# Kernel optimization log

Measured on AMD Instinct MI355X. Metric: run time of the kernel, lower is better.

## Reference

```python
import jax, jax.numpy as jnp
import numpy as np

EMBED_DIM = 768
ATTN_DIM = 64


def setup_inputs() -> dict:
    key = jax.random.key(0)
    k1, k2, k3, k4 = jax.random.split(key, 4)
    embedded = jax.random.normal(k1, (4, 4096, EMBED_DIM), dtype=jnp.float32)
    # nn.Linear(embed, attn, bias=False).weight has shape [attn, embed]; y = x @ W.T
    scale = 1.0 / np.sqrt(EMBED_DIM)
    Wq = jax.random.uniform(k2, (ATTN_DIM, EMBED_DIM), dtype=jnp.float32, minval=-scale, maxval=scale)
    Wk = jax.random.uniform(k3, (ATTN_DIM, EMBED_DIM), dtype=jnp.float32, minval=-scale, maxval=scale)
    Wv = jax.random.uniform(k4, (ATTN_DIM, EMBED_DIM), dtype=jnp.float32, minval=-scale, maxval=scale)
    return {"embedded": embedded, "Wq": Wq, "Wk": Wk, "Wv": Wv}


def reference(embedded, Wq, Wk, Wv):
    # Q, K, V: [b, s, a]
    Q = jnp.einsum('bse,ae->bsa', embedded, Wq)
    K = jnp.einsum('bse,ae->bsa', embedded, Wk)
    V = jnp.einsum('bse,ae->bsa', embedded, Wv)
    attn_dim = K.shape[2]
    scores = jnp.einsum('bqa,bka->bqk', Q, K) / jnp.sqrt(jnp.float32(attn_dim))
    s = scores.shape[1]
    # causal mask: positions above the diagonal get -inf
    causal = jnp.tril(jnp.ones((s, s), dtype=bool))
    scores = jnp.where(causal, scores, -jnp.inf)
    probs = jax.nn.softmax(scores, axis=2)
    out = jnp.einsum('bqk,bka->bqa', probs, V)
    return jnp.round(out, 4)
```

## Files before the change

kernel.cpp:

```cpp
#include <hip/hip_runtime.h>
#include <hip/hip_bf16.h>
#include <math.h>

#define EMBED  768
#define SEQ    4096
#define ADIM   64
#define NBATCH 4
#define QSCALE (0.125f * 1.44269504088896340736f)

typedef __bf16 bf16;
typedef unsigned int u32;
typedef __attribute__((ext_vector_type(8))) __bf16 bf16x8;
typedef __attribute__((ext_vector_type(4))) __bf16 bf16x4;
typedef __attribute__((ext_vector_type(4))) float f32x4;
typedef __attribute__((ext_vector_type(16))) float f32x16;

__device__ __forceinline__ f32x4 mfma16(bf16x8 a, bf16x8 b, f32x4 c) {
  return __builtin_amdgcn_mfma_f32_16x16x32_bf16(a, b, c, 0, 0, 0);
}
__device__ __forceinline__ f32x16 mfma32(bf16x8 a, bf16x8 b, f32x16 c) {
  return __builtin_amdgcn_mfma_f32_32x32x16_bf16(a, b, c, 0, 0, 0);
}
__device__ __forceinline__ unsigned cvtpk(float lo, float hi) {
  unsigned d;
  asm("v_cvt_pk_bf16_f32 %0, %1, %2" : "=v"(d) : "v"(lo), "v"(hi));
  return d;
}
__device__ __forceinline__ void gl_lds16(const bf16* g, bf16* l) {
  __builtin_amdgcn_global_load_lds(
      (const __attribute__((address_space(1))) u32*)g,
      (__attribute__((address_space(3))) u32*)l, 16, 0, 0);
}

__global__ __launch_bounds__(256, 4) void proj_kernel(
    const float* __restrict__ x,
    const float* __restrict__ Wq, const float* __restrict__ Wk,
    const float* __restrict__ Wv,
    bf16* __restrict__ Qs, bf16* __restrict__ Ks, bf16* __restrict__ Vt)
{
  __shared__ bf16 Wl[2][192][40];
  __shared__ bf16 Xl[2][32][40];

  const int t    = threadIdx.x;
  const int lane = t & 63;
  const int w    = t >> 6;
  const int band = w >> 1;
  const int half = w & 1;
  const int r    = lane & 15;
  const int g    = lane >> 4;
  const long long row0 = (long long)blockIdx.x * 32;

  f32x4 acc[6];
  #pragma unroll
  for (int i = 0; i < 6; ++i) acc[i] = f32x4{0.f, 0.f, 0.f, 0.f};

  const int wrow = t >> 2;
  const int wg   = t & 3;
  const long long woff = (long long)wrow * EMBED + wg * 8;
  const float* wqs = Wq + woff;
  const float* wks = Wk + woff;
  const float* wvs = Wv + woff;
  const int xrow = t >> 3;
  const int xcol = (t & 7) * 4;
  const float* xsrc = x + (row0 + xrow) * EMBED + xcol;

  #define WWRITE(buf, base, va, vb, sc)                                      \
    {                                                                        \
      uint2 p0, p1;                                                          \
      p0.x = cvtpk(va.x * sc, va.y * sc);                                    \
      p0.y = cvtpk(va.z * sc, va.w * sc);                                    \
      p1.x = cvtpk(vb.x * sc, vb.y * sc);                                    \
      p1.y = cvtpk(vb.z * sc, vb.w * sc);                                    \
      *reinterpret_cast<uint2*>(&Wl[buf][(base) + wrow][wg * 8])     = p0;   \
      *reinterpret_cast<uint2*>(&Wl[buf][(base) + wrow][wg * 8 + 4]) = p1;   \
    }

  {
    float4 qa = *reinterpret_cast<const float4*>(wqs);
    float4 qb = *reinterpret_cast<const float4*>(wqs + 4);
    float4 ka = *reinterpret_cast<const float4*>(wks);
    float4 kb = *reinterpret_cast<const float4*>(wks + 4);
    float4 va = *reinterpret_cast<const float4*>(wvs);
    float4 vb = *reinterpret_cast<const float4*>(wvs + 4);
    float4 xv = *reinterpret_cast<const float4*>(xsrc);
    WWRITE(0, 0,   qa, qb, QSCALE);
    WWRITE(0, 64,  ka, kb, 1.0f);
    WWRITE(0, 128, va, vb, 1.0f);
    uint2 xp; xp.x = cvtpk(xv.x, xv.y); xp.y = cvtpk(xv.z, xv.w);
    *reinterpret_cast<uint2*>(&Xl[0][xrow][xcol]) = xp;
  }
  float4 xv_n = *reinterpret_cast<const float4*>(xsrc + 32);
  __syncthreads();

  int cur = 0;
  for (int kt = 0; kt < 24; ++kt) {
    float4 qa, qb, ka, kb, va, vb, xv_n2;
    const bool pfW = kt < 23;
    if (pfW) {
      const int k0n = (kt + 1) * 32;
      qa = *reinterpret_cast<const float4*>(wqs + k0n);
      qb = *reinterpret_cast<const float4*>(wqs + k0n + 4);
      ka = *reinterpret_cast<const float4*>(wks + k0n);
      kb = *reinterpret_cast<const float4*>(wks + k0n + 4);
      va = *reinterpret_cast<const float4*>(wvs + k0n);
      vb = *reinterpret_cast<const float4*>(wvs + k0n + 4);
    }
    if (kt < 22)
      xv_n2 = *reinterpret_cast<const float4*>(xsrc + (kt + 2) * 32);

    bf16x8 af = *reinterpret_cast<const bf16x8*>(&Xl[cur][band * 16 + r][g * 8]);
    #pragma unroll
    for (int i = 0; i < 6; ++i) {
      const int n = half * 6 + i;
      bf16x8 bfrag = *reinterpret_cast<const bf16x8*>(&Wl[cur][n * 16 + r][g * 8]);
      acc[i] = mfma16(af, bfrag, acc[i]);
    }

    if (pfW) {
      WWRITE(cur ^ 1, 0,   qa, qb, QSCALE);
      WWRITE(cur ^ 1, 64,  ka, kb, 1.0f);
      WWRITE(cur ^ 1, 128, va, vb, 1.0f);
      uint2 xp; xp.x = cvtpk(xv_n.x, xv_n.y); xp.y = cvtpk(xv_n.z, xv_n.w);
      *reinterpret_cast<uint2*>(&Xl[cur ^ 1][xrow][xcol]) = xp;
    }
    xv_n = xv_n2;
    __syncthreads();
    cur ^= 1;
  }
  #undef WWRITE

  const long long rowbase = row0 + band * 16 + g * 4;
  const int bb = (int)(rowbase >> 12);
  const int ss = (int)(rowbase & 4095);
  #pragma unroll
  for (int i = 0; i < 6; ++i) {
    const int gt = half * 6 + i;
    if (gt < 4) {
      #pragma unroll
      for (int j = 0; j < 4; ++j)
        Qs[(rowbase + j) * ADIM + gt * 16 + r] = (bf16)(acc[i][j]);
    } else if (gt < 8) {
      #pragma unroll
      for (int j = 0; j < 4; ++j)
        Ks[(rowbase + j) * ADIM + (gt - 4) * 16 + r] = (bf16)(acc[i][j]);
    } else {
      const int d = (gt - 8) * 16 + r;
      bf16x4 pack;
      pack[0] = (bf16)(acc[i][0]); pack[1] = (bf16)(acc[i][1]);
      pack[2] = (bf16)(acc[i][2]); pack[3] = (bf16)(acc[i][3]);
      *reinterpret_cast<bf16x4*>(
          &Vt[(((long long)bb * 128 + (ss >> 5)) * 64 + d) * 32 + (ss & 31)]) = pack;
    }
  }
}

__global__ __launch_bounds__(768) void attn_kernel(
    const bf16* __restrict__ Qs, const bf16* __restrict__ Ks,
    const bf16* __restrict__ Vt, float* __restrict__ out)
{
  __shared__ bf16 Kst[12][2048];
  __shared__ bf16 Vst[12][2048];
  __shared__ unsigned short OldsU[12][32][72];
  __shared__ float Llds[12][32];

  const int t    = threadIdx.x;
  const int lane = t & 63;
  const int w    = t >> 6;
  const int q    = lane & 31;
  const int h    = lane >> 5;
  const int bi   = blockIdx.x;
  const int b    = bi & 3;
  const int p    = bi >> 2;

  const bf16* Qb = Qs + (long long)b * SEQ * ADIM;
  const bf16* Kb = Ks + (long long)b * SEQ * ADIM;
  const bf16* Vb = Vt + (long long)b * SEQ * ADIM;

  const int Ri = lane >> 3;
  const int ci = lane & 7;
  const bf16* kdma = Kb + (long long)Ri * ADIM + (ci ^ Ri) * 8;
  bf16* kslot = &Kst[w][0];
  const int vd = lane >> 2;
  const int vc = lane & 3;
  const bf16* vdma = Vb + (long long)vd * 32 + ((vc ^ (vd & 3)) * 8);
  bf16* vslot = &Vst[w][0];

  const char* kbase = (const char*)kslot;
  const bf16x8* kfp0 = (const bf16x8*)(kbase + q * 128 + (((0 + h) ^ (q & 7)) << 4));
  const bf16x8* kfp1 = (const bf16x8*)(kbase + q * 128 + (((2 + h) ^ (q & 7)) << 4));
  const bf16x8* kfp2 = (const bf16x8*)(kbase + q * 128 + (((4 + h) ^ (q & 7)) << 4));
  const bf16x8* kfp3 = (const bf16x8*)(kbase + q * 128 + (((6 + h) ^ (q & 7)) << 4));
  const char* vbase = (const char*)vslot;
  const bf16x8* vfp00 = (const bf16x8*)(vbase + q * 64        + (((0 + h) ^ (q & 3)) << 4));
  const bf16x8* vfp01 = (const bf16x8*)(vbase + q * 64        + (((2 + h) ^ (q & 3)) << 4));
  const bf16x8* vfp10 = (const bf16x8*)(vbase + 2048 + q * 64 + (((0 + h) ^ (q & 3)) << 4));
  const bf16x8* vfp11 = (const bf16x8*)(vbase + 2048 + q * 64 + (((2 + h) ^ (q & 3)) << 4));

  #define KVDMA(st_)                                                         \
    {                                                                        \
      const bf16* ksrc = kdma + (long long)((st_) * 32) * ADIM;              \
      gl_lds16(ksrc,             kslot);                                     \
      gl_lds16(ksrc +  8 * ADIM, kslot + 512);                               \
      gl_lds16(ksrc + 16 * ADIM, kslot + 1024);                              \
      gl_lds16(ksrc + 24 * ADIM, kslot + 1536);                              \
      const bf16* vsrc = vdma + (long long)(st_) * 2048;                     \
      gl_lds16(vsrc,        vslot);                                          \
      gl_lds16(vsrc +  512, vslot + 512);                                    \
      gl_lds16(vsrc + 1024, vslot + 1024);                                   \
      gl_lds16(vsrc + 1536, vslot + 1536);                                   \
    }

  for (int ti = 0; ti < 2; ++ti) {
    const int qt = ti ? (127 - p) : p;
    const int qb = qt * 32;

    if (w <= qt) KVDMA(w);

    bf16x8 qf[4];
    #pragma unroll
    for (int kc = 0; kc < 4; ++kc)
      qf[kc] = *reinterpret_cast<const bf16x8*>(Qb + (qb + q) * ADIM + kc * 16 + h * 8);

    f32x16 o0 = {0,0,0,0,0,0,0,0,0,0,0,0,0,0,0,0};
    f32x16 o1 = {0,0,0,0,0,0,0,0,0,0,0,0,0,0,0,0};
    float l = 0.f;

    for (int st = w; st <= qt; st += 12) {
      const int kv0 = st * 32;

      asm volatile("s_waitcnt vmcnt(0)" ::: "memory");
      __builtin_amdgcn_sched_barrier(0);

      bf16x8 kf0 = *kfp0, kf1 = *kfp1, kf2 = *kfp2, kf3 = *kfp3;
      bf16x8 vf00 = *vfp00, vf01 = *vfp01, vf10 = *vfp10, vf11 = *vfp11;
      asm volatile("s_waitcnt lgkmcnt(0)" ::: "memory");
      __builtin_amdgcn_sched_barrier(0);
      if (st + 12 <= qt) KVDMA(st + 12);
      __builtin_amdgcn_sched_barrier(0);

      f32x16 s = {0,0,0,0,0,0,0,0,0,0,0,0,0,0,0,0};
      __builtin_amdgcn_s_setprio(1);
      s = mfma32(kf0, qf[0], s);
      s = mfma32(kf1, qf[1], s);
      s = mfma32(kf2, qf[2], s);
      s = mfma32(kf3, qf[3], s);
      __builtin_amdgcn_s_setprio(0);

      if (st == qt) {
        #pragma unroll
        for (int i = 0; i < 4; ++i)
          #pragma unroll
          for (int j = 0; j < 4; ++j)
            if (kv0 + j + 8 * i + 4 * h > qb + q) s[i * 4 + j] = -INFINITY;
      }

      float rs = 0.f;
      #pragma unroll
      for (int rr = 0; rr < 16; ++rr) { s[rr] = exp2f(s[rr]); rs += s[rr]; }
      l += rs;

      {
        unsigned a0 = cvtpk(s[0], s[1]), a1 = cvtpk(s[2], s[3]);
        unsigned b0 = cvtpk(s[4], s[5]), b1 = cvtpk(s[6], s[7]);
        unsigned a0x = __shfl_xor((int)a0, 32), a1x = __shfl_xor((int)a1, 32);
        unsigned b0x = __shfl_xor((int)b0, 32), b1x = __shfl_xor((int)b1, 32);
        union { unsigned u[4]; bf16x8 v; } pa0;
        pa0.u[0] = h ? b0x : a0;  pa0.u[1] = h ? b1x : a1;
        pa0.u[2] = h ? b0  : a0x; pa0.u[3] = h ? b1  : a1x;
        __builtin_amdgcn_s_setprio(1);
        o0 = mfma32(vf00, pa0.v, o0);
        o1 = mfma32(vf10, pa0.v, o1);
        __builtin_amdgcn_s_setprio(0);
      }
      {
        unsigned c0 = cvtpk(s[8],  s[9]),  c1 = cvtpk(s[10], s[11]);
        unsigned d0 = cvtpk(s[12], s[13]), d1 = cvtpk(s[14], s[15]);
        unsigned c0x = __shfl_xor((int)c0, 32), c1x = __shfl_xor((int)c1, 32);
        unsigned d0x = __shfl_xor((int)d0, 32), d1x = __shfl_xor((int)d1, 32);
        union { unsigned u[4]; bf16x8 v; } pa1;
        pa1.u[0] = h ? d0x : c0;  pa1.u[1] = h ? d1x : c1;
        pa1.u[2] = h ? d0  : c0x; pa1.u[3] = h ? d1  : c1x;
        __builtin_amdgcn_s_setprio(1);
        o0 = mfma32(vf01, pa1.v, o0);
        o1 = mfma32(vf11, pa1.v, o1);
        __builtin_amdgcn_s_setprio(0);
      }
    }

    #pragma unroll
    for (int r2 = 0; r2 < 4; ++r2) {
      uint2 u0, u1;
      u0.x = cvtpk(o0[r2*4+0], o0[r2*4+1]); u0.y = cvtpk(o0[r2*4+2], o0[r2*4+3]);
      u1.x = cvtpk(o1[r2*4+0], o1[r2*4+1]); u1.y = cvtpk(o1[r2*4+2], o1[r2*4+3]);
      *reinterpret_cast<uint2*>(&OldsU[w][q][8 * r2 + 4 * h])      = u0;
      *reinterpret_cast<uint2*>(&OldsU[w][q][32 + 8 * r2 + 4 * h]) = u1;
    }
    const float lt = l + __shfl_xor(l, 32);
    if (h == 0) Llds[w][q] = lt;
    __syncthreads();

    if (t < 512) {
      const int cq = t >> 4;
      const int cd = (t & 15) * 4;
      float lf = 0.f;
      float o4[4] = {0.f, 0.f, 0.f, 0.f};
      #pragma unroll
      for (int w2 = 0; w2 < 12; ++w2) {
        lf += Llds[w2][cq];
        const uint2 uv = *reinterpret_cast<const uint2*>(&OldsU[w2][cq][cd]);
        o4[0] += __uint_as_float(uv.x << 16);
        o4[1] += __uint_as_float(uv.x & 0xffff0000u);
        o4[2] += __uint_as_float(uv.y << 16);
        o4[3] += __uint_as_float(uv.y & 0xffff0000u);
      }
      const float inv = 1.f / lf;
      float4 res;
      res.x = o4[0] * inv; res.y = o4[1] * inv;
      res.z = o4[2] * inv; res.w = o4[3] * inv;
      *reinterpret_cast<float4*>(out + ((long long)b * SEQ + qb + cq) * ADIM + cd) = res;
    }
    __syncthreads();
  }
  #undef KVDMA
}

extern "C" void kernel_launch(void* const* d_in, const int* in_sizes, int n_in,
                              void* d_out, int out_size, void* d_ws, size_t ws_size,
                              hipStream_t stream) {
  const float* x  = (const float*)d_in[0];
  const float* Wq = (const float*)d_in[1];
  const float* Wk = (const float*)d_in[2];
  const float* Wv = (const float*)d_in[3];

  const size_t qkvElems = (size_t)NBATCH * SEQ * ADIM;
  bf16* Qs = (bf16*)d_ws;
  bf16* Ks = Qs + qkvElems;
  bf16* Vt = Ks + qkvElems;

  proj_kernel<<<NBATCH * SEQ / 32, 256, 0, stream>>>(x, Wq, Wk, Wv, Qs, Ks, Vt);
  attn_kernel<<<256, 768, 0, stream>>>(Qs, Ks, Vt, (float*)d_out);
}
```

Baseline: 47.61 us.

## Double projection tile to 64 rows with 512 threads to reuse weight tiles

The projection kernel now processes 64 rows per block with 512 threads instead of 32 rows with 256. Each weight tile loaded into LDS is shared by twice as many rows, which halves how often the weights are re-read and converted across the grid. Staging is simplified so each thread loads one float4 each of Wq, Wk, Wv and x per k-step. The x prefetch is reduced from two steps ahead to one, which may expose more global latency, and the larger block may lower occupancy.

Result: slower. 56.24 us (+18.1%).

```diff
diff --git a/kernel.cpp b/kernel.cpp
--- a/kernel.cpp
+++ b/kernel.cpp
@@ -32,14 +32,14 @@
       (__attribute__((address_space(3))) u32*)l, 16, 0, 0);
 }
 
-__global__ __launch_bounds__(256, 4) void proj_kernel(
+__global__ __launch_bounds__(512, 4) void proj_kernel(
     const float* __restrict__ x,
     const float* __restrict__ Wq, const float* __restrict__ Wk,
     const float* __restrict__ Wv,
     bf16* __restrict__ Qs, bf16* __restrict__ Ks, bf16* __restrict__ Vt)
 {
   __shared__ bf16 Wl[2][192][40];
-  __shared__ bf16 Xl[2][32][40];
+  __shared__ bf16 Xl[2][64][40];
 
   const int t    = threadIdx.x;
   const int lane = t & 63;
@@ -48,65 +48,54 @@
   const int half = w & 1;
   const int r    = lane & 15;
   const int g    = lane >> 4;
-  const long long row0 = (long long)blockIdx.x * 32;
+  const long long row0 = (long long)blockIdx.x * 64;
 
   f32x4 acc[6];
   #pragma unroll
   for (int i = 0; i < 6; ++i) acc[i] = f32x4{0.f, 0.f, 0.f, 0.f};
 
-  const int wrow = t >> 2;
-  const int wg   = t & 3;
-  const long long woff = (long long)wrow * EMBED + wg * 8;
-  const float* wqs = Wq + woff;
-  const float* wks = Wk + woff;
-  const float* wvs = Wv + woff;
-  const int xrow = t >> 3;
-  const int xcol = (t & 7) * 4;
-  const float* xsrc = x + (row0 + xrow) * EMBED + xcol;
-
-  #define WWRITE(buf, base, va, vb, sc)                                      \
+  const int srow = t >> 3;
+  const int scol = (t & 7) * 4;
+  const long long soff = (long long)srow * EMBED + scol;
+  const float* wqs  = Wq + soff;
+  const float* wks  = Wk + soff;
+  const float* wvs  = Wv + soff;
+  const float* xsrc = x + (row0 + srow) * EMBED + scol;
+
+  #define WX_WRITE(buf, qa, ka, va, xv)                                      \
     {                                                                        \
-      uint2 p0, p1;                                                          \
-      p0.x = cvtpk(va.x * sc, va.y * sc);                                    \
-      p0.y = cvtpk(va.z * sc, va.w * sc);                                    \
-      p1.x = cvtpk(vb.x * sc, vb.y * sc);                                    \
-      p1.y = cvtpk(vb.z * sc, vb.w * sc);                                    \
-      *reinterpret_cast<uint2*>(&Wl[buf][(base) + wrow][wg * 8])     = p0;   \
-      *reinterpret_cast<uint2*>(&Wl[buf][(base) + wrow][wg * 8 + 4]) = p1;   \
+      uint2 p;                                                               \
+      p.x = cvtpk(qa.x * QSCALE, qa.y * QSCALE);                             \
+      p.y = cvtpk(qa.z * QSCALE, qa.w * QSCALE);                             \
+      *reinterpret_cast<uint2*>(&Wl[buf][srow][scol]) = p;                   \
+      p.x = cvtpk(ka.x, ka.y); p.y = cvtpk(ka.z, ka.w);                      \
+      *reinterpret_cast<uint2*>(&Wl[buf][64 + srow][scol]) = p;              \
+      p.x = cvtpk(va.x, va.y); p.y = cvtpk(va.z, va.w);                      \
+      *reinterpret_cast<uint2*>(&Wl[buf][128 + srow][scol]) = p;             \
+      p.x = cvtpk(xv.x, xv.y); p.y = cvtpk(xv.z, xv.w);                      \
+      *reinterpret_cast<uint2*>(&Xl[buf][srow][scol]) = p;                   \
     }
 
   {
     float4 qa = *reinterpret_cast<const float4*>(wqs);
-    float4 qb = *reinterpret_cast<const float4*>(wqs + 4);
     float4 ka = *reinterpret_cast<const float4*>(wks);
-    float4 kb = *reinterpret_cast<const float4*>(wks + 4);
     float4 va = *reinterpret_cast<const float4*>(wvs);
-    float4 vb = *reinterpret_cast<const float4*>(wvs + 4);
     float4 xv = *reinterpret_cast<const float4*>(xsrc);
-    WWRITE(0, 0,   qa, qb, QSCALE);
-    WWRITE(0, 64,  ka, kb, 1.0f);
-    WWRITE(0, 128, va, vb, 1.0f);
-    uint2 xp; xp.x = cvtpk(xv.x, xv.y); xp.y = cvtpk(xv.z, xv.w);
-    *reinterpret_cast<uint2*>(&Xl[0][xrow][xcol]) = xp;
+    WX_WRITE(0, qa, ka, va, xv);
   }
-  float4 xv_n = *reinterpret_cast<const float4*>(xsrc + 32);
   __syncthreads();
 
   int cur = 0;
   for (int kt = 0; kt < 24; ++kt) {
-    float4 qa, qb, ka, kb, va, vb, xv_n2;
-    const bool pfW = kt < 23;
-    if (pfW) {
+    float4 qa, ka, va, xv;
+    const bool pf = kt < 23;
+    if (pf) {
       const int k0n = (kt + 1) * 32;
       qa = *reinterpret_cast<const float4*>(wqs + k0n);
-      qb = *reinterpret_cast<const float4*>(wqs + k0n + 4);
       ka = *reinterpret_cast<const float4*>(wks + k0n);
-      kb = *reinterpret_cast<const float4*>(wks + k0n + 4);
       va = *reinterpret_cast<const float4*>(wvs + k0n);
-      vb = *reinterpret_cast<const float4*>(wvs + k0n + 4);
-    }
-    if (kt < 22)
-      xv_n2 = *reinterpret_cast<const float4*>(xsrc + (kt + 2) * 32);
+      xv = *reinterpret_cast<const float4*>(xsrc + k0n);
+    }
 
     bf16x8 af = *reinterpret_cast<const bf16x8*>(&Xl[cur][band * 16 + r][g * 8]);
     #pragma unroll
@@ -116,18 +105,11 @@
       acc[i] = mfma16(af, bfrag, acc[i]);
     }
 
-    if (pfW) {
-      WWRITE(cur ^ 1, 0,   qa, qb, QSCALE);
-      WWRITE(cur ^ 1, 64,  ka, kb, 1.0f);
-      WWRITE(cur ^ 1, 128, va, vb, 1.0f);
-      uint2 xp; xp.x = cvtpk(xv_n.x, xv_n.y); xp.y = cvtpk(xv_n.z, xv_n.w);
-      *reinterpret_cast<uint2*>(&Xl[cur ^ 1][xrow][xcol]) = xp;
-    }
-    xv_n = xv_n2;
+    if (pf) WX_WRITE(cur ^ 1, qa, ka, va, xv);
     __syncthreads();
     cur ^= 1;
   }
-  #undef WWRITE
+  #undef WX_WRITE
 
   const long long rowbase = row0 + band * 16 + g * 4;
   const int bb = (int)(rowbase >> 12);
@@ -337,6 +319,6 @@
   bf16* Ks = Qs + qkvElems;
   bf16* Vt = Ks + qkvElems;
 
-  proj_kernel<<<NBATCH * SEQ / 32, 256, 0, stream>>>(x, Wq, Wk, Wv, Qs, Ks, Vt);
+  proj_kernel<<<NBATCH * SEQ / 64, 512, 0, stream>>>(x, Wq, Wk, Wv, Qs, Ks, Vt);
   attn_kernel<<<256, 768, 0, stream>>>(Qs, Ks, Vt, (float*)d_out);
 }
```
